# Performance work log

Hardware: AMD Instinct MI355X
Metric: run time of the kernel (lower is better)

Reference implementation:

```python
import jax, jax.numpy as jnp
import numpy as np

B, H, S, D = 2, 16, 2048, 64
POLAR_SCALE = 0.125
QJL_SCALE = 0.01


def setup_inputs() -> dict:
    key = jax.random.key(0)
    ks = jax.random.split(key, 5)
    shape = (B, H, S, D)
    return {
        "q": jax.random.normal(ks[0], shape, dtype=jnp.float32),
        "k_polar": jax.random.normal(ks[1], shape, dtype=jnp.float32),
        "k_qjl": jax.random.normal(ks[2], shape, dtype=jnp.float32),
        "v_polar": jax.random.normal(ks[3], shape, dtype=jnp.float32),
        "v_qjl": jax.random.normal(ks[4], shape, dtype=jnp.float32),
    }


def reference(q, k_polar, k_qjl, v_polar, v_qjl):
    head_dim = q.shape[-1]
    sm_scale = 1.0 / np.sqrt(head_dim).astype(np.float32)
    # fused dequant of K/V from polar + qjl codes
    k = k_polar * POLAR_SCALE + k_qjl * QJL_SCALE  # [B,H,S,D]
    v = v_polar * POLAR_SCALE + v_qjl * QJL_SCALE  # [B,H,S,D]
    # non-causal attention with online-softmax-equivalent stable softmax
    scores = jnp.einsum("bhsd,bhtd->bhst", q * sm_scale, k)  # [B,H,S,S]
    p = jax.nn.softmax(scores, axis=-1)
    out = jnp.einsum("bhst,bhtd->bhsd", p, v)
    return out
```

## Files before the change

### kernel.cpp

```cpp
#include <hip/hip_runtime.h>

#define SS 2048
#define DD 64
#define NBH 32
#define KVB 64
#define BQ 128
#define NIT (SS / KVB)

typedef __attribute__((ext_vector_type(4))) float f32x4;
typedef __attribute__((ext_vector_type(4))) float float4_t;
typedef __attribute__((ext_vector_type(4))) short bf16x4;
typedef __attribute__((ext_vector_type(8))) short bf16x8;
typedef __attribute__((ext_vector_type(2))) unsigned int u32x2;

typedef const __attribute__((address_space(1))) unsigned int gu32_t;
typedef __attribute__((address_space(3))) unsigned int lu32_t;

__device__ __forceinline__ unsigned short f2bf(float f) {
  unsigned u = __builtin_bit_cast(unsigned, f);
  u += 0x7fffu + ((u >> 16) & 1u);
  return (unsigned short)(u >> 16);
}

__device__ __forceinline__ unsigned cvt_pk_bf16(float lo, float hi) {
  unsigned r;
  asm("v_cvt_pk_bf16_f32 %0, %1, %2" : "=v"(r) : "v"(lo), "v"(hi));
  return r;
}

__device__ __forceinline__ f32x4 MFMA32(bf16x8 a, bf16x8 b, f32x4 c) {
  return __builtin_amdgcn_mfma_f32_16x16x32_bf16(a, b, c, 0, 0, 0);
}

#if __has_builtin(__builtin_amdgcn_mfma_f32_16x16x16bf16_1k)
__device__ __forceinline__ f32x4 MFMA16(bf16x4 a, bf16x4 b, f32x4 c) {
  return __builtin_amdgcn_mfma_f32_16x16x16bf16_1k(a, b, c, 0, 0, 0);
}
#else
__device__ __forceinline__ f32x4 MFMA16(bf16x4 a, bf16x4 b, f32x4 c) {
  asm("v_mfma_f32_16x16x16_bf16 %0, %1, %2, %0" : "+v"(c) : "v"(a), "v"(b));
  return c;
}
#endif

__global__ void dequant_k_kernel(const float* __restrict__ kp,
                                 const float* __restrict__ kq,
                                 unsigned short* __restrict__ Kd) {
  int i = (blockIdx.x * 256 + threadIdx.x) * 4;
  float4_t a = *(const float4_t*)(kp + i);
  float4_t b = *(const float4_t*)(kq + i);
  bf16x4 r;
#pragma unroll
  for (int j = 0; j < 4; ++j)
    r[j] = (short)f2bf(a[j] * 0.125f + b[j] * 0.01f);
  *(bf16x4*)(Kd + i) = r;
}

__global__ void dequant_vt_kernel(const float* __restrict__ vp,
                                  const float* __restrict__ vq,
                                  unsigned short* __restrict__ Vt) {
  __shared__ unsigned short lds[64 * 68];
  int bh = blockIdx.x >> 5;
  int sbase = (blockIdx.x & 31) * 64;
  int t = threadIdx.x;
#pragma unroll
  for (int p = 0; p < 4; ++p) {
    int s = p * 16 + (t >> 4);
    int d4 = (t & 15) * 4;
    size_t gi = ((size_t)bh * SS + sbase + s) * DD + d4;
    float4_t a = *(const float4_t*)(vp + gi);
    float4_t b = *(const float4_t*)(vq + gi);
    bf16x4 r;
#pragma unroll
    for (int j = 0; j < 4; ++j)
      r[j] = (short)f2bf(a[j] * 0.125f + b[j] * 0.01f);
    *(bf16x4*)&lds[s * 68 + d4] = r;
  }
  __syncthreads();
#pragma unroll
  for (int p = 0; p < 2; ++p) {
    int c = p * 256 + t;
    int d = c >> 3;
    int sc = (c & 7) * 8;
    bf16x8 r;
#pragma unroll
    for (int j = 0; j < 8; ++j)
      r[j] = (short)lds[(sc + j) * 68 + d];
    *(bf16x8*)(Vt + ((size_t)bh * DD + d) * SS + sbase + sc) = r;
  }
}

__global__ __launch_bounds__(256, 2) void attn_kernel(
    const float* __restrict__ q,
    const unsigned short* __restrict__ Kd,
    const unsigned short* __restrict__ Vt,
    float* __restrict__ out) {
  __shared__ unsigned short ldsK[2][KVB * DD];
  __shared__ unsigned short ldsV[2][DD * KVB];

  int bid = blockIdx.x;
  int vb = (bid & 7) * 64 + (bid >> 3);
  int bh = vb >> 4;
  int qbase = (vb & 15) * BQ;
  int t = threadIdx.x;
  int lane = t & 63;
  int w = t >> 6;
  int g = lane >> 4;
  int qi = lane & 15;

  const unsigned short* kg = Kd + (size_t)bh * SS * DD;
  const unsigned short* vg = Vt + (size_t)bh * DD * SS;

  const unsigned short* gsK[2];
  const unsigned short* gsV[2];
  int ldso[2];
#pragma unroll
  for (int p = 0; p < 2; ++p) {
    int cc = p * 256 + t;
    int row = cc >> 3;
    int slot = (cc & 7) ^ (row & 7);
    gsK[p] = kg + (size_t)row * DD + slot * 8;
    gsV[p] = vg + (size_t)row * SS + slot * 8;
    ldso[p] = cc * 16;
  }

  auto stage = [&](int it, int b) {
#pragma unroll
    for (int p = 0; p < 2; ++p)
      __builtin_amdgcn_global_load_lds(
          (gu32_t*)(gsK[p] + (size_t)it * (KVB * DD)),
          (lu32_t*)((char*)(&ldsK[b][0]) + ldso[p]), 16, 0, 0);
#pragma unroll
    for (int p = 0; p < 2; ++p)
      __builtin_amdgcn_global_load_lds(
          (gu32_t*)(gsV[p] + it * KVB),
          (lu32_t*)((char*)(&ldsV[b][0]) + ldso[p]), 16, 0, 0);
  };

  stage(0, 0);

  const float QSCALE = 0.125f * 1.44269504088896f;

  bf16x8 qf[2][2];
  const float* qp = q + ((size_t)bh * SS + qbase + w * 32) * DD;
#pragma unroll
  for (int qt = 0; qt < 2; ++qt)
#pragma unroll
    for (int kc = 0; kc < 2; ++kc) {
      const float* p0 = qp + (qt * 16 + qi) * DD + kc * 32 + g * 8;
      float4_t a = *(const float4_t*)(p0);
      float4_t b = *(const float4_t*)(p0 + 4);
      bf16x8 f;
#pragma unroll
      for (int j = 0; j < 4; ++j) {
        f[j] = (short)f2bf(a[j] * QSCALE);
        f[j + 4] = (short)f2bf(b[j] * QSCALE);
      }
      qf[qt][kc] = f;
    }

  f32x4 oacc[2][4];
#pragma unroll
  for (int qt = 0; qt < 2; ++qt)
#pragma unroll
    for (int dt = 0; dt < 4; ++dt) oacc[qt][dt] = f32x4{0.f, 0.f, 0.f, 0.f};
  float m[2] = {-3.0e38f, -3.0e38f};
  float lsum[2] = {0.f, 0.f};

  __syncthreads();

  for (int it = 0; it < NIT; ++it) {
    int cur = it & 1;
    if (it + 1 < NIT) stage(it + 1, cur ^ 1);

    const char* bK = (const char*)&ldsK[cur][0];
    const char* bV = (const char*)&ldsV[cur][0];

    f32x4 sacc[2][4];
#pragma unroll
    for (int qt = 0; qt < 2; ++qt)
#pragma unroll
      for (int mt = 0; mt < 4; ++mt) sacc[qt][mt] = f32x4{0.f, 0.f, 0.f, 0.f};
#pragma unroll
    for (int mt = 0; mt < 4; ++mt) {
      int row = mt * 16 + qi;
#pragma unroll
      for (int kc = 0; kc < 2; ++kc) {
        int colb = (kc * 64 + g * 16) ^ ((row & 7) << 4);
        bf16x8 kf = *(const bf16x8*)(bK + row * 128 + colb);
        sacc[0][mt] = MFMA32(kf, qf[0][kc], sacc[0][mt]);
        sacc[1][mt] = MFMA32(kf, qf[1][kc], sacc[1][mt]);
      }
    }

    bf16x4 pf[2][4];
#pragma unroll
    for (int qt = 0; qt < 2; ++qt) {
      float t0 = fmaxf(fmaxf(sacc[qt][0][0], sacc[qt][0][1]),
                       fmaxf(sacc[qt][0][2], sacc[qt][0][3]));
      float t1 = fmaxf(fmaxf(sacc[qt][1][0], sacc[qt][1][1]),
                       fmaxf(sacc[qt][1][2], sacc[qt][1][3]));
      float t2 = fmaxf(fmaxf(sacc[qt][2][0], sacc[qt][2][1]),
                       fmaxf(sacc[qt][2][2], sacc[qt][2][3]));
      float t3 = fmaxf(fmaxf(sacc[qt][3][0], sacc[qt][3][1]),
                       fmaxf(sacc[qt][3][2], sacc[qt][3][3]));
      float tm = fmaxf(fmaxf(t0, t1), fmaxf(t2, t3));
      tm = fmaxf(tm, __shfl_xor(tm, 16));
      tm = fmaxf(tm, __shfl_xor(tm, 32));
      if (!__all(tm <= m[qt] + 8.0f)) {
        float mn = fmaxf(m[qt], tm);
        float sc = __builtin_amdgcn_exp2f(m[qt] - mn);
        m[qt] = mn;
        lsum[qt] *= sc;
#pragma unroll
        for (int dt = 0; dt < 4; ++dt) oacc[qt][dt] *= sc;
      }
      float mn = m[qt];
      float ps = 0.f;
#pragma unroll
      for (int mt = 0; mt < 4; ++mt) {
        float p0 = __builtin_amdgcn_exp2f(sacc[qt][mt][0] - mn);
        float p1 = __builtin_amdgcn_exp2f(sacc[qt][mt][1] - mn);
        float p2 = __builtin_amdgcn_exp2f(sacc[qt][mt][2] - mn);
        float p3 = __builtin_amdgcn_exp2f(sacc[qt][mt][3] - mn);
        ps += (p0 + p1) + (p2 + p3);
        u32x2 pk = {cvt_pk_bf16(p0, p1), cvt_pk_bf16(p2, p3)};
        pf[qt][mt] = __builtin_bit_cast(bf16x4, pk);
      }
      ps += __shfl_xor(ps, 16);
      ps += __shfl_xor(ps, 32);
      lsum[qt] += ps;
    }

#pragma unroll
    for (int dt = 0; dt < 4; ++dt) {
      int row = dt * 16 + qi;
#pragma unroll
      for (int mt = 0; mt < 4; ++mt) {
        int colb = (mt * 32 + g * 8) ^ ((row & 7) << 4);
        bf16x4 vf = *(const bf16x4*)(bV + row * 128 + colb);
        oacc[0][dt] = MFMA16(vf, pf[0][mt], oacc[0][dt]);
        oacc[1][dt] = MFMA16(vf, pf[1][mt], oacc[1][dt]);
      }
    }
    __syncthreads();
  }

  float* op = out + ((size_t)bh * SS + qbase + w * 32) * DD;
#pragma unroll
  for (int qt = 0; qt < 2; ++qt) {
    float rl = 1.0f / lsum[qt];
#pragma unroll
    for (int dt = 0; dt < 4; ++dt) {
      f32x4 o = oacc[qt][dt] * rl;
      *(f32x4*)(op + (qt * 16 + qi) * DD + dt * 16 + g * 4) = o;
    }
  }
}

extern "C" void kernel_launch(void* const* d_in, const int* in_sizes, int n_in,
                              void* d_out, int out_size, void* d_ws, size_t ws_size,
                              hipStream_t stream) {
  const float* q  = (const float*)d_in[0];
  const float* kp = (const float*)d_in[1];
  const float* kq = (const float*)d_in[2];
  const float* vp = (const float*)d_in[3];
  const float* vq = (const float*)d_in[4];
  float* out = (float*)d_out;

  unsigned short* Kd = (unsigned short*)d_ws;
  unsigned short* Vt = Kd + (size_t)NBH * SS * DD;

  dequant_k_kernel<<<4096, 256, 0, stream>>>(kp, kq, Kd);
  dequant_vt_kernel<<<1024, 256, 0, stream>>>(vp, vq, Vt);
  attn_kernel<<<512, 256, 0, stream>>>(q, Kd, Vt, out);
}
```

Measured before the change: 179.6 us.

## Use 8 waves per block with one 16-row query tile each

The attention kernel goes from 4 waves handling two 16-row query tiles each to 8 waves (512 threads) handling one 16-row tile each, with launch bounds raised to 512 threads. Each thread now issues one global-to-LDS load per stage instead of two, and per-wave register use for accumulators and Q fragments is halved. The aim is more resident waves to hide LDS and MFMA latency. The cost is that each K/V LDS fragment is now read by twice as many waves, with less MFMA reuse per load, and there are more waves per block barrier.

```diff
diff --git a/kernel.cpp b/kernel.cpp
--- a/kernel.cpp
+++ b/kernel.cpp
@@ -90,7 +90,7 @@
   }
 }
 
-__global__ __launch_bounds__(256, 2) void attn_kernel(
+__global__ __launch_bounds__(512, 4) void attn_kernel(
     const float* __restrict__ q,
     const unsigned short* __restrict__ Kd,
     const unsigned short* __restrict__ Vt,
@@ -111,61 +111,46 @@
   const unsigned short* kg = Kd + (size_t)bh * SS * DD;
   const unsigned short* vg = Vt + (size_t)bh * DD * SS;
 
-  const unsigned short* gsK[2];
-  const unsigned short* gsV[2];
-  int ldso[2];
-#pragma unroll
-  for (int p = 0; p < 2; ++p) {
-    int cc = p * 256 + t;
-    int row = cc >> 3;
-    int slot = (cc & 7) ^ (row & 7);
-    gsK[p] = kg + (size_t)row * DD + slot * 8;
-    gsV[p] = vg + (size_t)row * SS + slot * 8;
-    ldso[p] = cc * 16;
-  }
+  int srow = t >> 3;
+  int slot = (t & 7) ^ (srow & 7);
+  const unsigned short* gsK = kg + (size_t)srow * DD + slot * 8;
+  const unsigned short* gsV = vg + (size_t)srow * SS + slot * 8;
+  int ldso = t * 16;
 
   auto stage = [&](int it, int b) {
-#pragma unroll
-    for (int p = 0; p < 2; ++p)
-      __builtin_amdgcn_global_load_lds(
-          (gu32_t*)(gsK[p] + (size_t)it * (KVB * DD)),
-          (lu32_t*)((char*)(&ldsK[b][0]) + ldso[p]), 16, 0, 0);
-#pragma unroll
-    for (int p = 0; p < 2; ++p)
-      __builtin_amdgcn_global_load_lds(
-          (gu32_t*)(gsV[p] + it * KVB),
-          (lu32_t*)((char*)(&ldsV[b][0]) + ldso[p]), 16, 0, 0);
+    __builtin_amdgcn_global_load_lds(
+        (gu32_t*)(gsK + (size_t)it * (KVB * DD)),
+        (lu32_t*)((char*)(&ldsK[b][0]) + ldso), 16, 0, 0);
+    __builtin_amdgcn_global_load_lds(
+        (gu32_t*)(gsV + it * KVB),
+        (lu32_t*)((char*)(&ldsV[b][0]) + ldso), 16, 0, 0);
   };
 
   stage(0, 0);
 
   const float QSCALE = 0.125f * 1.44269504088896f;
 
-  bf16x8 qf[2][2];
-  const float* qp = q + ((size_t)bh * SS + qbase + w * 32) * DD;
-#pragma unroll
-  for (int qt = 0; qt < 2; ++qt)
-#pragma unroll
-    for (int kc = 0; kc < 2; ++kc) {
-      const float* p0 = qp + (qt * 16 + qi) * DD + kc * 32 + g * 8;
-      float4_t a = *(const float4_t*)(p0);
-      float4_t b = *(const float4_t*)(p0 + 4);
-      bf16x8 f;
-#pragma unroll
-      for (int j = 0; j < 4; ++j) {
-        f[j] = (short)f2bf(a[j] * QSCALE);
-        f[j + 4] = (short)f2bf(b[j] * QSCALE);
-      }
-      qf[qt][kc] = f;
-    }
-
-  f32x4 oacc[2][4];
-#pragma unroll
-  for (int qt = 0; qt < 2; ++qt)
-#pragma unroll
-    for (int dt = 0; dt < 4; ++dt) oacc[qt][dt] = f32x4{0.f, 0.f, 0.f, 0.f};
-  float m[2] = {-3.0e38f, -3.0e38f};
-  float lsum[2] = {0.f, 0.f};
+  bf16x8 qf[2];
+  const float* qp = q + ((size_t)bh * SS + qbase + w * 16 + qi) * DD;
+#pragma unroll
+  for (int kc = 0; kc < 2; ++kc) {
+    const float* p0 = qp + kc * 32 + g * 8;
+    float4_t a = *(const float4_t*)(p0);
+    float4_t b = *(const float4_t*)(p0 + 4);
+    bf16x8 f;
+#pragma unroll
+    for (int j = 0; j < 4; ++j) {
+      f[j] = (short)f2bf(a[j] * QSCALE);
+      f[j + 4] = (short)f2bf(b[j] * QSCALE);
+    }
+    qf[kc] = f;
+  }
+
+  f32x4 oacc[4];
+#pragma unroll
+  for (int dt = 0; dt < 4; ++dt) oacc[dt] = f32x4{0.f, 0.f, 0.f, 0.f};
+  float m = -3.0e38f;
+  float lsum = 0.f;
 
   __syncthreads();
 
@@ -176,11 +161,9 @@
     const char* bK = (const char*)&ldsK[cur][0];
     const char* bV = (const char*)&ldsV[cur][0];
 
-    f32x4 sacc[2][4];
-#pragma unroll
-    for (int qt = 0; qt < 2; ++qt)
-#pragma unroll
-      for (int mt = 0; mt < 4; ++mt) sacc[qt][mt] = f32x4{0.f, 0.f, 0.f, 0.f};
+    f32x4 sacc[4];
+#pragma unroll
+    for (int mt = 0; mt < 4; ++mt) sacc[mt] = f32x4{0.f, 0.f, 0.f, 0.f};
 #pragma unroll
     for (int mt = 0; mt < 4; ++mt) {
       int row = mt * 16 + qi;
@@ -188,48 +171,42 @@
       for (int kc = 0; kc < 2; ++kc) {
         int colb = (kc * 64 + g * 16) ^ ((row & 7) << 4);
         bf16x8 kf = *(const bf16x8*)(bK + row * 128 + colb);
-        sacc[0][mt] = MFMA32(kf, qf[0][kc], sacc[0][mt]);
-        sacc[1][mt] = MFMA32(kf, qf[1][kc], sacc[1][mt]);
-      }
-    }
-
-    bf16x4 pf[2][4];
-#pragma unroll
-    for (int qt = 0; qt < 2; ++qt) {
-      float t0 = fmaxf(fmaxf(sacc[qt][0][0], sacc[qt][0][1]),
-                       fmaxf(sacc[qt][0][2], sacc[qt][0][3]));
-      float t1 = fmaxf(fmaxf(sacc[qt][1][0], sacc[qt][1][1]),
-                       fmaxf(sacc[qt][1][2], sacc[qt][1][3]));
-      float t2 = fmaxf(fmaxf(sacc[qt][2][0], sacc[qt][2][1]),
-                       fmaxf(sacc[qt][2][2], sacc[qt][2][3]));
-      float t3 = fmaxf(fmaxf(sacc[qt][3][0], sacc[qt][3][1]),
-                       fmaxf(sacc[qt][3][2], sacc[qt][3][3]));
+        sacc[mt] = MFMA32(kf, qf[kc], sacc[mt]);
+      }
+    }
+
+    bf16x4 pf[4];
+    {
+      float t0 = fmaxf(fmaxf(sacc[0][0], sacc[0][1]), fmaxf(sacc[0][2], sacc[0][3]));
+      float t1 = fmaxf(fmaxf(sacc[1][0], sacc[1][1]), fmaxf(sacc[1][2], sacc[1][3]));
+      float t2 = fmaxf(fmaxf(sacc[2][0], sacc[2][1]), fmaxf(sacc[2][2], sacc[2][3]));
+      float t3 = fmaxf(fmaxf(sacc[3][0], sacc[3][1]), fmaxf(sacc[3][2], sacc[3][3]));
       float tm = fmaxf(fmaxf(t0, t1), fmaxf(t2, t3));
       tm = fmaxf(tm, __shfl_xor(tm, 16));
       tm = fmaxf(tm, __shfl_xor(tm, 32));
-      if (!__all(tm <= m[qt] + 8.0f)) {
-        float mn = fmaxf(m[qt], tm);
-        float sc = __builtin_amdgcn_exp2f(m[qt] - mn);
-        m[qt] = mn;
-        lsum[qt] *= sc;
-#pragma unroll
-        for (int dt = 0; dt < 4; ++dt) oacc[qt][dt] *= sc;
-      }
-      float mn = m[qt];
+      if (!__all(tm <= m + 8.0f)) {
+        float mn = fmaxf(m, tm);
+        float sc = __builtin_amdgcn_exp2f(m - mn);
+        m = mn;
+        lsum *= sc;
+#pragma unroll
+        for (int dt = 0; dt < 4; ++dt) oacc[dt] *= sc;
+      }
+      float mn = m;
       float ps = 0.f;
 #pragma unroll
       for (int mt = 0; mt < 4; ++mt) {
-        float p0 = __builtin_amdgcn_exp2f(sacc[qt][mt][0] - mn);
-        float p1 = __builtin_amdgcn_exp2f(sacc[qt][mt][1] - mn);
-        float p2 = __builtin_amdgcn_exp2f(sacc[qt][mt][2] - mn);
-        float p3 = __builtin_amdgcn_exp2f(sacc[qt][mt][3] - mn);
+        float p0 = __builtin_amdgcn_exp2f(sacc[mt][0] - mn);
+        float p1 = __builtin_amdgcn_exp2f(sacc[mt][1] - mn);
+        float p2 = __builtin_amdgcn_exp2f(sacc[mt][2] - mn);
+        float p3 = __builtin_amdgcn_exp2f(sacc[mt][3] - mn);
         ps += (p0 + p1) + (p2 + p3);
         u32x2 pk = {cvt_pk_bf16(p0, p1), cvt_pk_bf16(p2, p3)};
-        pf[qt][mt] = __builtin_bit_cast(bf16x4, pk);
+        pf[mt] = __builtin_bit_cast(bf16x4, pk);
       }
       ps += __shfl_xor(ps, 16);
       ps += __shfl_xor(ps, 32);
-      lsum[qt] += ps;
+      lsum += ps;
     }
 
 #pragma unroll
@@ -239,22 +216,18 @@
       for (int mt = 0; mt < 4; ++mt) {
         int colb = (mt * 32 + g * 8) ^ ((row & 7) << 4);
         bf16x4 vf = *(const bf16x4*)(bV + row * 128 + colb);
-        oacc[0][dt] = MFMA16(vf, pf[0][mt], oacc[0][dt]);
-        oacc[1][dt] = MFMA16(vf, pf[1][mt], oacc[1][dt]);
+        oacc[dt] = MFMA16(vf, pf[mt], oacc[dt]);
       }
     }
     __syncthreads();
   }
 
-  float* op = out + ((size_t)bh * SS + qbase + w * 32) * DD;
-#pragma unroll
-  for (int qt = 0; qt < 2; ++qt) {
-    float rl = 1.0f / lsum[qt];
-#pragma unroll
-    for (int dt = 0; dt < 4; ++dt) {
-      f32x4 o = oacc[qt][dt] * rl;
-      *(f32x4*)(op + (qt * 16 + qi) * DD + dt * 16 + g * 4) = o;
-    }
+  float* op = out + ((size_t)bh * SS + qbase + w * 16 + qi) * DD;
+  float rl = 1.0f / lsum;
+#pragma unroll
+  for (int dt = 0; dt < 4; ++dt) {
+    f32x4 o = oacc[dt] * rl;
+    *(f32x4*)(op + dt * 16 + g * 4) = o;
   }
 }
 
@@ -273,5 +246,5 @@
 
   dequant_k_kernel<<<4096, 256, 0, stream>>>(kp, kq, Kd);
   dequant_vt_kernel<<<1024, 256, 0, stream>>>(vp, vq, Vt);
-  attn_kernel<<<512, 256, 0, stream>>>(q, Kd, Vt, out);
-}
+  attn_kernel<<<512, 512, 0, stream>>>(q, Kd, Vt, out);
+}
```

After: 175.8 us. 2.1% less time.
